# Kernel tuning notes

Measured on AMD Instinct MI355X. Metric: run time of the kernel, lower is better.

## Reference

```python
import jax, jax.numpy as jnp
import numpy as np


def setup_inputs() -> dict:
    key = jax.random.key(0)
    k1, = jax.random.split(key, 1)
    N, C, A, R = 8, 4, 180, 180
    hough_map = jax.random.normal(k1, (N, C, A, R), dtype=jnp.float32)
    mask_width = jnp.full((1,), 3.0, dtype=jnp.float32)
    return {"hough_map": hough_map, "mask_width": mask_width, "H": 256, "W": 256}


def _peak_mask(hough_map):
    # 3x3 stride-1 same-padded max pool (torch pads with -inf for max_pool2d)
    pooled = jax.lax.reduce_window(
        hough_map, -jnp.inf, jax.lax.max,
        window_dimensions=(1, 1, 3, 3), window_strides=(1, 1, 1, 1), padding='SAME')
    mx = jnp.max(hough_map, axis=(2, 3), keepdims=True)
    return (hough_map == pooled) & (hough_map > 0.5 * mx)  # [N,C,A,R] bool


def reference(hough_map, mask_width, H, W):
    N, C, A, R = hough_map.shape
    peaks = _peak_mask(hough_map)                      # [N,C,A,R]
    # pixel grid centered at image center
    xc = jnp.arange(W, dtype=jnp.float32) - (W - 1) / 2.0   # [W]
    yc = jnp.arange(H, dtype=jnp.float32) - (H - 1) / 2.0   # [H]
    max_rho = np.sqrt((W / 2) ** 2 + (H / 2) ** 2)
    delta_rho = 2.0 * max_rho / (R - 1)
    r_phys = (jnp.arange(R, dtype=jnp.float32) - (R - 1) / 2.0) * delta_rho  # [R]
    thetas = jnp.arange(A, dtype=jnp.float32) * (np.pi / A)
    cos_t, sin_t = jnp.cos(thetas), jnp.sin(thetas)
    peaks_a = jnp.transpose(peaks, (2, 0, 1, 3)).astype(jnp.float32)  # [A,N,C,R]

    def step(acc, xs):
        ct, st, pk = xs                                 # scalars, [N,C,R]
        r_est = xc[None, :] * ct + yc[:, None] * st     # [H,W]
        # indicator: pixel lies within mask_width of rho-bin r at this angle
        ind = (jnp.abs(r_est[:, :, None] - r_phys) < mask_width[0]).astype(jnp.float32)  # [H,W,R]
        contrib = jnp.einsum('hwr,ncr->nchw', ind, pk)  # >0 iff any peak covers pixel
        acc = jnp.maximum(acc, (contrib > 0).astype(jnp.float32))
        return acc, None

    acc0 = jnp.zeros((N, C, H, W), dtype=jnp.float32)
    out, _ = jax.lax.scan(step, acc0, (cos_t, sin_t, peaks_a))
    return out
```

## Files before the change

### kernel.cpp

```cpp
#include <hip/hip_runtime.h>
#include <math.h>

#define A_  180
#define R_  180
#define NC  32
#define AR  32400
#define NW  508
#define NBK 127
#define CAPL 1024
#define ROWS_PB 8
#define SL  32

typedef unsigned long long u64;
typedef unsigned int u32;

#define OFF_PMAX 0
#define OFF_TBL  16384
#define OFF_CM   20480

__device__ __forceinline__ float probe_d(int u, float ct2, float yst, float rp) {
  return __fsub_rn(__fadd_rn(__fmul_rn(__fsub_rn((float)u, 127.5f), ct2), yst), rp);
}

__global__ __launch_bounds__(256) void cand_kernel(
    const float* __restrict__ hm,
    const int* __restrict__ Hp, const int* __restrict__ Wp,
    float* __restrict__ pmax, u64* __restrict__ candmask,
    float* __restrict__ tbl) {
  int bx = blockIdx.x, nc = blockIdx.y;
  int tid = threadIdx.x;
  if (bx == NBK) {
    if (nc != 0) return;
    int H = Hp[0], W = Wp[0];
    double max_rho = sqrt((double)(W/2)*(double)(W/2) + (double)(H/2)*(double)(H/2));
    float drho = (float)(2.0 * max_rho / (double)(R_ - 1));
    if (tid < A_) {
      float theta = __fmul_rn((float)tid, (float)(3.14159265358979323846 / (double)A_));
      tbl[tid]        = (float)cos((double)theta);
      tbl[A_ + tid]   = (float)sin((double)theta);
      tbl[2*A_ + tid] = __fmul_rn(__fsub_rn((float)tid, (float)((R_-1)*0.5)), drho);
    }
    return;
  }
  const float* base = hm + (size_t)nc * AR;
  int idx = bx * 256 + tid;
  bool lm = false;
  float val = -INFINITY;
  if (idx < AR) {
    val = base[idx];
    int a = idx / R_;
    int r = idx - a * R_;
    float mx = -INFINITY;
    #pragma unroll
    for (int da = -1; da <= 1; ++da) {
      #pragma unroll
      for (int dr = -1; dr <= 1; ++dr) {
        if (da == 0 && dr == 0) continue;
        int aa = a + da, rr = r + dr;
        bool ok = (aa >= 0) && (aa < A_) && (rr >= 0) && (rr < R_);
        float nb = base[ok ? (aa * R_ + rr) : idx];
        mx = ok ? fmaxf(mx, nb) : mx;
      }
    }
    lm = !(mx > val);
  }
  u64 mb = __ballot(lm);
  if ((tid & 63) == 0)
    candmask[(size_t)nc * NW + bx * 4 + (tid >> 6)] = mb;

  float m = val;
  for (int off = 32; off; off >>= 1) m = fmaxf(m, __shfl_down(m, off, 64));
  __shared__ float sm[4];
  if ((tid & 63) == 0) sm[tid >> 6] = m;
  __syncthreads();
  if (tid == 0)
    pmax[nc * 128 + bx] = fmaxf(fmaxf(sm[0], sm[1]), fmaxf(sm[2], sm[3]));
}

__global__ __launch_bounds__(256) void raster_kernel(
    const float* __restrict__ hm, const float* __restrict__ mwp,
    const float* __restrict__ pmax, const u64* __restrict__ candmask,
    const float* __restrict__ tbl, float* __restrict__ out) {
  __shared__ float sct[A_], sst[A_], srp[A_];
  __shared__ float slct[CAPL], slst[CAPL], slrp[CAPL];
  __shared__ float smax[4];
  __shared__ u32 scnt;
  __shared__ u64 rowbits[ROWS_PB][4];
  int s   = blockIdx.x;
  int nc  = blockIdx.y;
  int tid = threadIdx.x;
  if (tid == 0) scnt = 0;
  if (tid < A_) {
    sct[tid] = tbl[tid]; sst[tid] = tbl[A_ + tid]; srp[tid] = tbl[2*A_ + tid];
  }
  float m = (tid < NBK) ? pmax[nc * 128 + tid] : -INFINITY;
  for (int off = 32; off; off >>= 1) m = fmaxf(m, __shfl_down(m, off, 64));
  if ((tid & 63) == 0) smax[tid >> 6] = m;
  __syncthreads();
  float thr = 0.5f * fmaxf(fmaxf(smax[0], smax[1]), fmaxf(smax[2], smax[3]));

  const float* base = hm + (size_t)nc * AR;
  const u64*   cm   = candmask + (size_t)nc * NW;
  for (int w = tid; w < NW; w += 256) {
    u64 bits = cm[w];
    while (bits) {
      int b = (int)__ffsll((long long)bits) - 1;
      bits &= bits - 1;
      int idx = (w << 6) + b;
      float val = base[idx];
      if (val > thr) {
        u32 slot = atomicAdd(&scnt, 1u);
        if (slot < CAPL) {
          int a = idx / R_;
          int r = idx - a * R_;
          slct[slot] = sct[a]; slst[slot] = sst[a]; slrp[slot] = srp[r];
        }
      }
    }
  }
  __syncthreads();
  int pc = (int)scnt; if (pc > CAPL) pc = CAPL;

  float mw  = mwp[0];
  float nmw = -mw;
  int row = tid >> 5;
  int sub = tid & (SL - 1);
  int y   = s * ROWS_PB + row;
  float ycv = __fsub_rn((float)y, 127.5f);

  u64 pm[4] = {0ull, 0ull, 0ull, 0ull};

  for (int i = sub; i < pc; i += SL) {
    float ct = slct[i], st = slst[i], rp = slrp[i];
    float ct2 = fabsf(ct);
    float yst = __fmul_rn(ycv, st);
    int u1, u2;
    if (ct2 >= 1e-3f) {
      float t   = rp - yst;
      float inv = __builtin_amdgcn_rcpf(ct2);
      float q1  = __fmaf_rn(t - mw, inv, 127.5f);
      float q2  = __fmaf_rn(t + mw, inv, 127.5f);
      q1 = fminf(fmaxf(q1, -2.0f), 260.0f);
      q2 = fminf(fmaxf(q2, -2.0f), 260.0f);
      int k1 = (int)ceilf(q1 - 0.5f); k1 = k1 < 0 ? 0 : (k1 > 255 ? 255 : k1);
      int k2 = (int)ceilf(q2 - 0.5f); k2 = k2 < 0 ? 0 : (k2 > 255 ? 255 : k2);
      float d1 = probe_d(k1, ct2, yst, rp);
      float d2 = probe_d(k2, ct2, yst, rp);
      u1 = k1 + ((d1 > nmw) ? 0 : 1);
      u2 = k2 + ((d2 >= mw) ? 0 : 1);
    } else {
      u1 = 0; u2 = 0;
      #pragma unroll
      for (int st2 = 256; st2; st2 >>= 1) {
        if (u1 + st2 <= 256) {
          float d = probe_d(u1 + st2 - 1, ct2, yst, rp);
          if (!(d > nmw)) u1 += st2;
        }
        if (u2 + st2 <= 256) {
          float d = probe_d(u2 + st2 - 1, ct2, yst, rp);
          if (!(d >= mw)) u2 += st2;
        }
      }
    }
    if (u1 < u2) {
      bool neg = ct < 0.0f;
      int xlo = neg ? 256 - u2 : u1;
      int xhi = neg ? 255 - u1 : u2 - 1;
      #pragma unroll
      for (int w = 0; w < 4; ++w) {
        int lo = xlo - (w << 6); lo = lo < 0 ? 0 : lo;
        int hi = xhi - (w << 6); hi = hi > 63 ? 63 : hi;
        if (lo <= hi) pm[w] |= (~0ull >> (63 - hi)) & (~0ull << lo);
      }
    }
  }

  #pragma unroll
  for (int mm = 1; mm < 32; mm <<= 1) {
    pm[0] |= __shfl_xor(pm[0], mm, 64);
    pm[1] |= __shfl_xor(pm[1], mm, 64);
    pm[2] |= __shfl_xor(pm[2], mm, 64);
    pm[3] |= __shfl_xor(pm[3], mm, 64);
  }
  if (sub < 4) {
    u64 v = (sub == 0) ? pm[0] : (sub == 1) ? pm[1] : (sub == 2) ? pm[2] : pm[3];
    rowbits[row][sub] = v;
  }
  __syncthreads();

  float* otile = out + (size_t)nc * 65536 + (size_t)s * ROWS_PB * 256;
  for (int j = tid; j < ROWS_PB * 64; j += 256) {
    int rr = j >> 6, c4 = j & 63;
    u64 wb = rowbits[rr][c4 >> 4];
    int sh = (c4 & 15) * 4;
    float4 v;
    v.x = (float)((wb >> sh) & 1ull);
    v.y = (float)((wb >> (sh + 1)) & 1ull);
    v.z = (float)((wb >> (sh + 2)) & 1ull);
    v.w = (float)((wb >> (sh + 3)) & 1ull);
    ((float4*)(otile + (size_t)rr * 256))[c4] = v;
  }
}

extern "C" void kernel_launch(void* const* d_in, const int* in_sizes, int n_in,
                              void* d_out, int out_size, void* d_ws, size_t ws_size,
                              hipStream_t stream) {
  const float* hm  = (const float*)d_in[0];
  const float* mwp = (const float*)d_in[1];
  const int*   Hp  = (const int*)d_in[2];
  const int*   Wp  = (const int*)d_in[3];
  float* out = (float*)d_out;

  char* base = (char*)d_ws;
  float* pmax = (float*)(base + OFF_PMAX);
  float* tbl  = (float*)(base + OFF_TBL);
  u64*   cm   = (u64*)(base + OFF_CM);

  cand_kernel<<<dim3(NBK + 1, NC), dim3(256), 0, stream>>>(
      hm, Hp, Wp, pmax, cm, tbl);

  raster_kernel<<<dim3(32, NC), dim3(256), 0, stream>>>(
      hm, mwp, pmax, cm, tbl, out);
}
```

Baseline: 47.53 us.

## Split peak filtering into separate kernel with wave-aggregated global compaction

Result: faster. 44.45 us (-6.5%).

```diff
diff --git a/kernel.cpp b/kernel.cpp
--- a/kernel.cpp
+++ b/kernel.cpp
@@ -7,7 +7,7 @@
 #define AR  32400
 #define NW  508
 #define NBK 127
-#define CAPL 1024
+#define CAP 1536
 #define ROWS_PB 8
 #define SL  32
 
@@ -16,7 +16,9 @@
 
 #define OFF_PMAX 0
 #define OFF_TBL  16384
-#define OFF_CM   20480
+#define OFF_CNT  20480
+#define OFF_CM   24576
+#define OFF_PD   154624
 
 __device__ __forceinline__ float probe_d(int u, float ct2, float yst, float rp) {
   return __fsub_rn(__fadd_rn(__fmul_rn(__fsub_rn((float)u, 127.5f), ct2), yst), rp);
@@ -26,11 +28,13 @@
     const float* __restrict__ hm,
     const int* __restrict__ Hp, const int* __restrict__ Wp,
     float* __restrict__ pmax, u64* __restrict__ candmask,
-    float* __restrict__ tbl) {
+    float* __restrict__ tbl, u32* __restrict__ cnt) {
   int bx = blockIdx.x, nc = blockIdx.y;
   int tid = threadIdx.x;
   if (bx == NBK) {
     if (nc != 0) return;
+    #pragma unroll
+    for (int k = 0; k < 4; ++k) cnt[k * 256 + tid] = 0u;
     int H = Hp[0], W = Wp[0];
     double max_rho = sqrt((double)(W/2)*(double)(W/2) + (double)(H/2)*(double)(H/2));
     float drho = (float)(2.0 * max_rho / (double)(R_ - 1));
@@ -77,61 +81,69 @@
     pmax[nc * 128 + bx] = fmaxf(fmaxf(sm[0], sm[1]), fmaxf(sm[2], sm[3]));
 }
 
-__global__ __launch_bounds__(256) void raster_kernel(
-    const float* __restrict__ hm, const float* __restrict__ mwp,
-    const float* __restrict__ pmax, const u64* __restrict__ candmask,
-    const float* __restrict__ tbl, float* __restrict__ out) {
-  __shared__ float sct[A_], sst[A_], srp[A_];
-  __shared__ float slct[CAPL], slst[CAPL], slrp[CAPL];
+__global__ __launch_bounds__(256) void filter_kernel(
+    const float* __restrict__ hm, const float* __restrict__ pmax,
+    const u64* __restrict__ candmask, const float* __restrict__ tbl,
+    u32* __restrict__ cnt, float4* __restrict__ pdata) {
+  int bx = blockIdx.x, nc = blockIdx.y;
+  int tid = threadIdx.x;
   __shared__ float smax[4];
-  __shared__ u32 scnt;
-  __shared__ u64 rowbits[ROWS_PB][4];
-  int s   = blockIdx.x;
-  int nc  = blockIdx.y;
-  int tid = threadIdx.x;
-  if (tid == 0) scnt = 0;
-  if (tid < A_) {
-    sct[tid] = tbl[tid]; sst[tid] = tbl[A_ + tid]; srp[tid] = tbl[2*A_ + tid];
-  }
   float m = (tid < NBK) ? pmax[nc * 128 + tid] : -INFINITY;
   for (int off = 32; off; off >>= 1) m = fmaxf(m, __shfl_down(m, off, 64));
   if ((tid & 63) == 0) smax[tid >> 6] = m;
   __syncthreads();
   float thr = 0.5f * fmaxf(fmaxf(smax[0], smax[1]), fmaxf(smax[2], smax[3]));
 
-  const float* base = hm + (size_t)nc * AR;
-  const u64*   cm   = candmask + (size_t)nc * NW;
-  for (int w = tid; w < NW; w += 256) {
-    u64 bits = cm[w];
-    while (bits) {
-      int b = (int)__ffsll((long long)bits) - 1;
-      bits &= bits - 1;
-      int idx = (w << 6) + b;
-      float val = base[idx];
-      if (val > thr) {
-        u32 slot = atomicAdd(&scnt, 1u);
-        if (slot < CAPL) {
-          int a = idx / R_;
-          int r = idx - a * R_;
-          slct[slot] = sct[a]; slst[slot] = sst[a]; slrp[slot] = srp[r];
-        }
-      }
-    }
-  }
-  __syncthreads();
-  int pc = (int)scnt; if (pc > CAPL) pc = CAPL;
+  int idx = bx * 256 + tid;
+  bool peak = false;
+  int a = 0, r = 0;
+  if (idx < AR) {
+    u64 w = candmask[(size_t)nc * NW + (idx >> 6)];
+    if ((w >> (idx & 63)) & 1ull) {
+      float val = hm[(size_t)nc * AR + idx];
+      if (val > thr) { peak = true; a = idx / R_; r = idx - a * R_; }
+    }
+  }
+  u64 mb = __ballot(peak);
+  if (mb) {
+    int lane = tid & 63;
+    int leader = (int)__ffsll((long long)mb) - 1;
+    u32 bslot = 0;
+    if (lane == leader) bslot = atomicAdd(&cnt[nc * 32], (u32)__popcll(mb));
+    bslot = (u32)__shfl((int)bslot, leader, 64);
+    if (peak) {
+      u32 slot = bslot + (u32)__popcll(mb & ((1ull << lane) - 1ull));
+      if (slot < CAP)
+        pdata[(size_t)nc * CAP + slot] =
+            make_float4(tbl[a], tbl[A_ + a], tbl[2 * A_ + r], 0.0f);
+    }
+  }
+}
+
+__global__ __launch_bounds__(256) void raster_kernel(
+    const float* __restrict__ mwp,
+    const u32* __restrict__ cntg, const float4* __restrict__ pdata,
+    float* __restrict__ out) {
+  __shared__ u64 rowbits[ROWS_PB][4];
+  int yb  = blockIdx.x;
+  int nc  = blockIdx.y;
+  int tid = threadIdx.x;
+  int row = tid >> 5;
+  int sub = tid & (SL - 1);
+
+  int cnt = (int)cntg[nc * 32]; if (cnt > CAP) cnt = CAP;
+  const float4* pdg = pdata + (size_t)nc * CAP;
 
   float mw  = mwp[0];
   float nmw = -mw;
-  int row = tid >> 5;
-  int sub = tid & (SL - 1);
-  int y   = s * ROWS_PB + row;
+  int   y   = yb * ROWS_PB + row;
   float ycv = __fsub_rn((float)y, 127.5f);
 
   u64 pm[4] = {0ull, 0ull, 0ull, 0ull};
 
-  for (int i = sub; i < pc; i += SL) {
-    float ct = slct[i], st = slst[i], rp = slrp[i];
+  for (int i = sub; i < cnt; i += SL) {
+    float4 pd = pdg[i];
+    float ct = pd.x, st = pd.y, rp = pd.z;
     float ct2 = fabsf(ct);
     float yst = __fmul_rn(ycv, st);
     int u1, u2;
@@ -188,7 +200,7 @@
   }
   __syncthreads();
 
-  float* otile = out + (size_t)nc * 65536 + (size_t)s * ROWS_PB * 256;
+  float* otile = out + (size_t)nc * 65536 + (size_t)yb * ROWS_PB * 256;
   for (int j = tid; j < ROWS_PB * 64; j += 256) {
     int rr = j >> 6, c4 = j & 63;
     u64 wb = rowbits[rr][c4 >> 4];
@@ -212,13 +224,17 @@
   float* out = (float*)d_out;
 
   char* base = (char*)d_ws;
-  float* pmax = (float*)(base + OFF_PMAX);
-  float* tbl  = (float*)(base + OFF_TBL);
-  u64*   cm   = (u64*)(base + OFF_CM);
+  float*  pmax = (float*)(base + OFF_PMAX);
+  float*  tbl  = (float*)(base + OFF_TBL);
+  u32*    cnt  = (u32*)(base + OFF_CNT);
+  u64*    cm   = (u64*)(base + OFF_CM);
+  float4* pdat = (float4*)(base + OFF_PD);
 
   cand_kernel<<<dim3(NBK + 1, NC), dim3(256), 0, stream>>>(
-      hm, Hp, Wp, pmax, cm, tbl);
-
-  raster_kernel<<<dim3(32, NC), dim3(256), 0, stream>>>(
-      hm, mwp, pmax, cm, tbl, out);
-}
+      hm, Hp, Wp, pmax, cm, tbl, cnt);
+
+  filter_kernel<<<dim3(NBK, NC), dim3(256), 0, stream>>>(
+      hm, pmax, cm, tbl, cnt, pdat);
+
+  raster_kernel<<<dim3(32, NC), dim3(256), 0, stream>>>(mwp, cnt, pdat, out);
+}
```

## Fuse candidate detection and rasterization into a single kernel

Applied to the files above, without the earlier changes.

After: 163.4 us. 3.44x slower.

```diff
diff --git a/kernel.cpp b/kernel.cpp
--- a/kernel.cpp
+++ b/kernel.cpp
@@ -5,114 +5,76 @@
 #define R_  180
 #define NC  32
 #define AR  32400
-#define NW  508
-#define NBK 127
-#define CAPL 1024
+#define CAPL 1536
 #define ROWS_PB 8
 #define SL  32
 
 typedef unsigned long long u64;
 typedef unsigned int u32;
 
-#define OFF_PMAX 0
-#define OFF_TBL  16384
-#define OFF_CM   20480
-
 __device__ __forceinline__ float probe_d(int u, float ct2, float yst, float rp) {
   return __fsub_rn(__fadd_rn(__fmul_rn(__fsub_rn((float)u, 127.5f), ct2), yst), rp);
 }
 
-__global__ __launch_bounds__(256) void cand_kernel(
-    const float* __restrict__ hm,
+__global__ __launch_bounds__(256) void mono_kernel(
+    const float* __restrict__ hm, const float* __restrict__ mwp,
     const int* __restrict__ Hp, const int* __restrict__ Wp,
-    float* __restrict__ pmax, u64* __restrict__ candmask,
-    float* __restrict__ tbl) {
-  int bx = blockIdx.x, nc = blockIdx.y;
+    float* __restrict__ out) {
+  int s   = blockIdx.x;
+  int nc  = blockIdx.y;
   int tid = threadIdx.x;
-  if (bx == NBK) {
-    if (nc != 0) return;
-    int H = Hp[0], W = Wp[0];
-    double max_rho = sqrt((double)(W/2)*(double)(W/2) + (double)(H/2)*(double)(H/2));
-    float drho = (float)(2.0 * max_rho / (double)(R_ - 1));
-    if (tid < A_) {
-      float theta = __fmul_rn((float)tid, (float)(3.14159265358979323846 / (double)A_));
-      tbl[tid]        = (float)cos((double)theta);
-      tbl[A_ + tid]   = (float)sin((double)theta);
-      tbl[2*A_ + tid] = __fmul_rn(__fsub_rn((float)tid, (float)((R_-1)*0.5)), drho);
-    }
-    return;
-  }
   const float* base = hm + (size_t)nc * AR;
-  int idx = bx * 256 + tid;
-  bool lm = false;
-  float val = -INFINITY;
-  if (idx < AR) {
-    val = base[idx];
-    int a = idx / R_;
-    int r = idx - a * R_;
-    float mx = -INFINITY;
-    #pragma unroll
-    for (int da = -1; da <= 1; ++da) {
-      #pragma unroll
-      for (int dr = -1; dr <= 1; ++dr) {
-        if (da == 0 && dr == 0) continue;
-        int aa = a + da, rr = r + dr;
-        bool ok = (aa >= 0) && (aa < A_) && (rr >= 0) && (rr < R_);
-        float nb = base[ok ? (aa * R_ + rr) : idx];
-        mx = ok ? fmaxf(mx, nb) : mx;
-      }
-    }
-    lm = !(mx > val);
-  }
-  u64 mb = __ballot(lm);
-  if ((tid & 63) == 0)
-    candmask[(size_t)nc * NW + bx * 4 + (tid >> 6)] = mb;
 
-  float m = val;
-  for (int off = 32; off; off >>= 1) m = fmaxf(m, __shfl_down(m, off, 64));
-  __shared__ float sm[4];
-  if ((tid & 63) == 0) sm[tid >> 6] = m;
-  __syncthreads();
-  if (tid == 0)
-    pmax[nc * 128 + bx] = fmaxf(fmaxf(sm[0], sm[1]), fmaxf(sm[2], sm[3]));
-}
-
-__global__ __launch_bounds__(256) void raster_kernel(
-    const float* __restrict__ hm, const float* __restrict__ mwp,
-    const float* __restrict__ pmax, const u64* __restrict__ candmask,
-    const float* __restrict__ tbl, float* __restrict__ out) {
   __shared__ float sct[A_], sst[A_], srp[A_];
   __shared__ float slct[CAPL], slst[CAPL], slrp[CAPL];
   __shared__ float smax[4];
   __shared__ u32 scnt;
   __shared__ u64 rowbits[ROWS_PB][4];
-  int s   = blockIdx.x;
-  int nc  = blockIdx.y;
-  int tid = threadIdx.x;
-  if (tid == 0) scnt = 0;
+  if (tid == 0) scnt = 0u;
+
   if (tid < A_) {
-    sct[tid] = tbl[tid]; sst[tid] = tbl[A_ + tid]; srp[tid] = tbl[2*A_ + tid];
+    int H = Hp[0], W = Wp[0];
+    double max_rho = sqrt((double)(W/2)*(double)(W/2) + (double)(H/2)*(double)(H/2));
+    float drho = (float)(2.0 * max_rho / (double)(R_ - 1));
+    float theta = __fmul_rn((float)tid, (float)(3.14159265358979323846 / (double)A_));
+    sct[tid] = (float)cos((double)theta);
+    sst[tid] = (float)sin((double)theta);
+    srp[tid] = __fmul_rn(__fsub_rn((float)tid, (float)((R_-1)*0.5)), drho);
   }
-  float m = (tid < NBK) ? pmax[nc * 128 + tid] : -INFINITY;
-  for (int off = 32; off; off >>= 1) m = fmaxf(m, __shfl_down(m, off, 64));
-  if ((tid & 63) == 0) smax[tid >> 6] = m;
+
+  {
+    const float4* p4 = (const float4*)base;
+    float m = -INFINITY;
+    for (int i = tid; i < AR / 4; i += 256) {
+      float4 v = p4[i];
+      m = fmaxf(fmaxf(m, fmaxf(v.x, v.y)), fmaxf(v.z, v.w));
+    }
+    for (int off = 32; off; off >>= 1) m = fmaxf(m, __shfl_down(m, off, 64));
+    if ((tid & 63) == 0) smax[tid >> 6] = m;
+  }
   __syncthreads();
   float thr = 0.5f * fmaxf(fmaxf(smax[0], smax[1]), fmaxf(smax[2], smax[3]));
 
-  const float* base = hm + (size_t)nc * AR;
-  const u64*   cm   = candmask + (size_t)nc * NW;
-  for (int w = tid; w < NW; w += 256) {
-    u64 bits = cm[w];
-    while (bits) {
-      int b = (int)__ffsll((long long)bits) - 1;
-      bits &= bits - 1;
-      int idx = (w << 6) + b;
-      float val = base[idx];
-      if (val > thr) {
+  for (int idx = tid; idx < AR; idx += 256) {
+    float val = base[idx];
+    if (val > thr) {
+      int a = idx / R_;
+      int r = idx - a * R_;
+      float mx = -INFINITY;
+      #pragma unroll
+      for (int da = -1; da <= 1; ++da) {
+        #pragma unroll
+        for (int dr = -1; dr <= 1; ++dr) {
+          if (da == 0 && dr == 0) continue;
+          int aa = a + da, rr = r + dr;
+          bool ok = (aa >= 0) && (aa < A_) && (rr >= 0) && (rr < R_);
+          float nb = base[ok ? (aa * R_ + rr) : idx];
+          mx = ok ? fmaxf(mx, nb) : mx;
+        }
+      }
+      if (!(mx > val)) {
         u32 slot = atomicAdd(&scnt, 1u);
         if (slot < CAPL) {
-          int a = idx / R_;
-          int r = idx - a * R_;
           slct[slot] = sct[a]; slst[slot] = sst[a]; slrp[slot] = srp[r];
         }
       }
@@ -211,14 +173,5 @@
   const int*   Wp  = (const int*)d_in[3];
   float* out = (float*)d_out;
 
-  char* base = (char*)d_ws;
-  float* pmax = (float*)(base + OFF_PMAX);
-  float* tbl  = (float*)(base + OFF_TBL);
-  u64*   cm   = (u64*)(base + OFF_CM);
-
-  cand_kernel<<<dim3(NBK + 1, NC), dim3(256), 0, stream>>>(
-      hm, Hp, Wp, pmax, cm, tbl);
-
-  raster_kernel<<<dim3(32, NC), dim3(256), 0, stream>>>(
-      hm, mwp, pmax, cm, tbl, out);
+  mono_kernel<<<dim3(32, NC), dim3(256), 0, stream>>>(hm, mwp, Hp, Wp, out);
 }
```

## Use one 1024-thread block per plane for peak gathering and rasterization

Applied to the files above, without the earlier changes.

New measurement: 146.0 us. 3.07x slower.

```diff
diff --git a/kernel.cpp b/kernel.cpp
--- a/kernel.cpp
+++ b/kernel.cpp
@@ -7,16 +7,13 @@
 #define AR  32400
 #define NW  508
 #define NBK 127
-#define CAPL 1024
-#define ROWS_PB 8
-#define SL  32
+#define CAPL 1536
 
 typedef unsigned long long u64;
 typedef unsigned int u32;
 
 #define OFF_PMAX 0
-#define OFF_TBL  16384
-#define OFF_CM   20480
+#define OFF_CM   16384
 
 __device__ __forceinline__ float probe_d(int u, float ct2, float yst, float rp) {
   return __fsub_rn(__fadd_rn(__fmul_rn(__fsub_rn((float)u, 127.5f), ct2), yst), rp);
@@ -24,24 +21,9 @@
 
 __global__ __launch_bounds__(256) void cand_kernel(
     const float* __restrict__ hm,
-    const int* __restrict__ Hp, const int* __restrict__ Wp,
-    float* __restrict__ pmax, u64* __restrict__ candmask,
-    float* __restrict__ tbl) {
+    float* __restrict__ pmax, u64* __restrict__ candmask) {
   int bx = blockIdx.x, nc = blockIdx.y;
   int tid = threadIdx.x;
-  if (bx == NBK) {
-    if (nc != 0) return;
-    int H = Hp[0], W = Wp[0];
-    double max_rho = sqrt((double)(W/2)*(double)(W/2) + (double)(H/2)*(double)(H/2));
-    float drho = (float)(2.0 * max_rho / (double)(R_ - 1));
-    if (tid < A_) {
-      float theta = __fmul_rn((float)tid, (float)(3.14159265358979323846 / (double)A_));
-      tbl[tid]        = (float)cos((double)theta);
-      tbl[A_ + tid]   = (float)sin((double)theta);
-      tbl[2*A_ + tid] = __fmul_rn(__fsub_rn((float)tid, (float)((R_-1)*0.5)), drho);
-    }
-    return;
-  }
   const float* base = hm + (size_t)nc * AR;
   int idx = bx * 256 + tid;
   bool lm = false;
@@ -77,42 +59,69 @@
     pmax[nc * 128 + bx] = fmaxf(fmaxf(sm[0], sm[1]), fmaxf(sm[2], sm[3]));
 }
 
-__global__ __launch_bounds__(256) void raster_kernel(
+__global__ __launch_bounds__(1024) void fr_kernel(
     const float* __restrict__ hm, const float* __restrict__ mwp,
+    const int* __restrict__ Hp, const int* __restrict__ Wp,
     const float* __restrict__ pmax, const u64* __restrict__ candmask,
-    const float* __restrict__ tbl, float* __restrict__ out) {
+    float* __restrict__ out) {
+  int nc  = blockIdx.x;
+  int tid = threadIdx.x;
+  const float* base = hm + (size_t)nc * AR;
+
   __shared__ float sct[A_], sst[A_], srp[A_];
   __shared__ float slct[CAPL], slst[CAPL], slrp[CAPL];
-  __shared__ float smax[4];
+  __shared__ float smax[16];
   __shared__ u32 scnt;
-  __shared__ u64 rowbits[ROWS_PB][4];
-  int s   = blockIdx.x;
-  int nc  = blockIdx.y;
-  int tid = threadIdx.x;
-  if (tid == 0) scnt = 0;
+  __shared__ u64 rowbits[256][4];
+  if (tid == 0) scnt = 0u;
+
   if (tid < A_) {
-    sct[tid] = tbl[tid]; sst[tid] = tbl[A_ + tid]; srp[tid] = tbl[2*A_ + tid];
-  }
-  float m = (tid < NBK) ? pmax[nc * 128 + tid] : -INFINITY;
-  for (int off = 32; off; off >>= 1) m = fmaxf(m, __shfl_down(m, off, 64));
-  if ((tid & 63) == 0) smax[tid >> 6] = m;
-  __syncthreads();
-  float thr = 0.5f * fmaxf(fmaxf(smax[0], smax[1]), fmaxf(smax[2], smax[3]));
-
-  const float* base = hm + (size_t)nc * AR;
-  const u64*   cm   = candmask + (size_t)nc * NW;
-  for (int w = tid; w < NW; w += 256) {
-    u64 bits = cm[w];
-    while (bits) {
-      int b = (int)__ffsll((long long)bits) - 1;
-      bits &= bits - 1;
-      int idx = (w << 6) + b;
-      float val = base[idx];
-      if (val > thr) {
-        u32 slot = atomicAdd(&scnt, 1u);
+    int H = Hp[0], W = Wp[0];
+    double max_rho = sqrt((double)(W/2)*(double)(W/2) + (double)(H/2)*(double)(H/2));
+    float drho = (float)(2.0 * max_rho / (double)(R_ - 1));
+    float theta = __fmul_rn((float)tid, (float)(3.14159265358979323846 / (double)A_));
+    sct[tid] = (float)cos((double)theta);
+    sst[tid] = (float)sin((double)theta);
+    srp[tid] = __fmul_rn(__fsub_rn((float)tid, (float)((R_-1)*0.5)), drho);
+  }
+
+  {
+    float m = (tid < NBK) ? pmax[nc * 128 + tid] : -INFINITY;
+    for (int off = 32; off; off >>= 1) m = fmaxf(m, __shfl_down(m, off, 64));
+    if ((tid & 63) == 0) smax[tid >> 6] = m;
+  }
+  __syncthreads();
+  float thr;
+  {
+    float mm = smax[0];
+    #pragma unroll
+    for (int k = 1; k < 16; ++k) mm = fmaxf(mm, smax[k]);
+    thr = 0.5f * mm;
+  }
+
+  const u64* cm = candmask + (size_t)nc * NW;
+  int lane = tid & 63;
+  #pragma unroll 4
+  for (int k = 0; k < 32; ++k) {
+    int idx = k * 1024 + tid;
+    bool peak = false;
+    int a = 0, r = 0;
+    if (idx < AR) {
+      u64 w = cm[idx >> 6];
+      if ((w >> (idx & 63)) & 1ull) {
+        float val = base[idx];
+        if (val > thr) { peak = true; a = idx / R_; r = idx - a * R_; }
+      }
+    }
+    u64 mb = __ballot(peak);
+    if (mb) {
+      int leader = (int)__ffsll((long long)mb) - 1;
+      u32 bslot = 0;
+      if (lane == leader) bslot = atomicAdd(&scnt, (u32)__popcll(mb));
+      bslot = (u32)__shfl((int)bslot, leader, 64);
+      if (peak) {
+        u32 slot = bslot + (u32)__popcll(mb & ((1ull << lane) - 1ull));
         if (slot < CAPL) {
-          int a = idx / R_;
-          int r = idx - a * R_;
           slct[slot] = sct[a]; slst[slot] = sst[a]; slrp[slot] = srp[r];
         }
       }
@@ -123,14 +132,13 @@
 
   float mw  = mwp[0];
   float nmw = -mw;
-  int row = tid >> 5;
-  int sub = tid & (SL - 1);
-  int y   = s * ROWS_PB + row;
-  float ycv = __fsub_rn((float)y, 127.5f);
+  int row = tid >> 2;
+  int sub = tid & 3;
+  float ycv = __fsub_rn((float)row, 127.5f);
 
   u64 pm[4] = {0ull, 0ull, 0ull, 0ull};
 
-  for (int i = sub; i < pc; i += SL) {
+  for (int i = sub; i < pc; i += 4) {
     float ct = slct[i], st = slst[i], rp = slrp[i];
     float ct2 = fabsf(ct);
     float yst = __fmul_rn(ycv, st);
@@ -176,20 +184,20 @@
   }
 
   #pragma unroll
-  for (int mm = 1; mm < 32; mm <<= 1) {
+  for (int mm = 1; mm < 4; mm <<= 1) {
     pm[0] |= __shfl_xor(pm[0], mm, 64);
     pm[1] |= __shfl_xor(pm[1], mm, 64);
     pm[2] |= __shfl_xor(pm[2], mm, 64);
     pm[3] |= __shfl_xor(pm[3], mm, 64);
   }
-  if (sub < 4) {
+  {
     u64 v = (sub == 0) ? pm[0] : (sub == 1) ? pm[1] : (sub == 2) ? pm[2] : pm[3];
     rowbits[row][sub] = v;
   }
   __syncthreads();
 
-  float* otile = out + (size_t)nc * 65536 + (size_t)s * ROWS_PB * 256;
-  for (int j = tid; j < ROWS_PB * 64; j += 256) {
+  float* oplane = out + (size_t)nc * 65536;
+  for (int j = tid; j < 16384; j += 1024) {
     int rr = j >> 6, c4 = j & 63;
     u64 wb = rowbits[rr][c4 >> 4];
     int sh = (c4 & 15) * 4;
@@ -198,7 +206,7 @@
     v.y = (float)((wb >> (sh + 1)) & 1ull);
     v.z = (float)((wb >> (sh + 2)) & 1ull);
     v.w = (float)((wb >> (sh + 3)) & 1ull);
-    ((float4*)(otile + (size_t)rr * 256))[c4] = v;
+    ((float4*)(oplane + (size_t)rr * 256))[c4] = v;
   }
 }
 
@@ -213,12 +221,10 @@
 
   char* base = (char*)d_ws;
   float* pmax = (float*)(base + OFF_PMAX);
-  float* tbl  = (float*)(base + OFF_TBL);
   u64*   cm   = (u64*)(base + OFF_CM);
 
-  cand_kernel<<<dim3(NBK + 1, NC), dim3(256), 0, stream>>>(
-      hm, Hp, Wp, pmax, cm, tbl);
-
-  raster_kernel<<<dim3(32, NC), dim3(256), 0, stream>>>(
-      hm, mwp, pmax, cm, tbl, out);
-}
+  cand_kernel<<<dim3(NBK, NC), dim3(256), 0, stream>>>(hm, pmax, cm);
+
+  fr_kernel<<<dim3(NC), dim3(1024), 0, stream>>>(
+      hm, mwp, Hp, Wp, pmax, cm, out);
+}
```
